# Kernel optimization log

Hardware: AMD Instinct MI355X
Metric: run time of the kernel (lower is better)

Reference implementation:

```python
import jax, jax.numpy as jnp
import numpy as np

EMBED_DIM = 1024
NUM_HEADS = 16
HEAD_DIM = EMBED_DIM // NUM_HEADS
LN_EPS = 1e-5


def setup_inputs() -> dict:
    key = jax.random.key(0)
    ks = jax.random.split(key, 6)
    b, s, d = 2, 2048, EMBED_DIM
    scale = 1.0 / np.sqrt(d)
    x = jax.random.normal(ks[0], (b, s, d), dtype=jnp.float32)
    w_qkv = jax.random.normal(ks[1], (d, 3 * d), dtype=jnp.float32) * scale
    b_qkv = jax.random.normal(ks[2], (3 * d,), dtype=jnp.float32) * 0.02
    w_out = jax.random.normal(ks[3], (d, d), dtype=jnp.float32) * scale
    b_out = jax.random.normal(ks[4], (d,), dtype=jnp.float32) * 0.02
    gamma = jnp.ones((d,), dtype=jnp.float32)
    ln_beta = jnp.zeros((d,), dtype=jnp.float32)
    beta = jax.random.normal(ks[5], (), dtype=jnp.float32) * 0.1
    return {"x": x, "w_qkv": w_qkv, "b_qkv": b_qkv, "w_out": w_out,
            "b_out": b_out, "gamma": gamma, "ln_beta": ln_beta, "beta": beta}


def _layernorm(x, gamma, ln_beta):
    mu = jnp.mean(x, axis=-1, keepdims=True)
    var = jnp.mean(jnp.square(x - mu), axis=-1, keepdims=True)
    return (x - mu) * jax.lax.rsqrt(var + LN_EPS) * gamma + ln_beta


def reference(x, w_qkv, b_qkv, w_out, b_out, gamma, ln_beta, beta):
    b, s, d = x.shape
    h, hd = NUM_HEADS, HEAD_DIM
    residual = x
    xn = _layernorm(x, gamma, ln_beta)
    qkv = xn @ w_qkv + b_qkv                       # [b, s, 3d]
    qkv = qkv.reshape(b, s, 3, h, hd)
    q = jnp.transpose(qkv[:, :, 0], (0, 2, 1, 3))  # [b, h, s, hd]
    k = jnp.transpose(qkv[:, :, 1], (0, 2, 1, 3))
    v = jnp.transpose(qkv[:, :, 2], (0, 2, 1, 3))
    attn = jnp.einsum('bhqd,bhkd->bhqk', q, k) / np.sqrt(hd)
    idx = jnp.arange(s)
    dist = jnp.abs(idx[None, :] - idx[:, None]).astype(attn.dtype)  # [s, s]
    attn = attn + beta * jnp.log1p(dist)[None, None, :, :]
    probs = jax.nn.softmax(attn, axis=-1)
    ctx = jnp.einsum('bhqk,bhkd->bhqd', probs, v)  # [b, h, s, hd]
    ctx = jnp.transpose(ctx, (0, 2, 1, 3)).reshape(b, s, d)
    return residual + ctx @ w_out + b_out
```

## Files before the change

kernel.cpp:

```cpp
#include <hip/hip_runtime.h>

#define SEQ 2048
#define DIM 1024
#define NHEAD 16
#define HDIM 64
#define NTOK 4096
#define N3D 3072

typedef __attribute__((ext_vector_type(8))) short bf16x8;
typedef __attribute__((ext_vector_type(4))) short bf16x4;
typedef __attribute__((ext_vector_type(4))) float floatx4;
typedef __attribute__((ext_vector_type(4))) unsigned short ushortx4;
typedef __attribute__((ext_vector_type(2))) int intx2;

__device__ __forceinline__ unsigned short f2bf(float f) {
    unsigned int u = __builtin_bit_cast(unsigned int, f);
    u += 0x7FFFu + ((u >> 16) & 1u);
    return (unsigned short)(u >> 16);
}

__device__ __forceinline__ unsigned int pack_bf16(float a, float b) {
    return (unsigned int)f2bf(a) | ((unsigned int)f2bf(b) << 16);
}

__device__ __forceinline__ void async_copy16(const void* g, const void* l) {
    __builtin_amdgcn_global_load_lds(
        (const __attribute__((address_space(1))) unsigned int*)(unsigned long long)g,
        (__attribute__((address_space(3))) unsigned int*)(unsigned int)(unsigned long long)l,
        16, 0, 0);
}

#define MFMA_BF16(a, b, c) __builtin_amdgcn_mfma_f32_16x16x32_bf16((a), (b), (c), 0, 0, 0)
#define MFMA16(a, b, c) __builtin_amdgcn_mfma_f32_16x16x16bf16_1k((a), (b), (c), 0, 0, 0)

__global__ __launch_bounds__(256)
void transpose_cvt(const float* __restrict__ src, unsigned short* __restrict__ dst,
                   int rows, int cols) {
    __shared__ float tile[32][33];
    const int c0 = blockIdx.x * 32, r0 = blockIdx.y * 32;
    const int tx = threadIdx.x & 31, ty = threadIdx.x >> 5;
    for (int i = 0; i < 4; ++i) {
        int r = ty + i * 8;
        tile[r][tx] = src[(size_t)(r0 + r) * cols + c0 + tx];
    }
    __syncthreads();
    for (int i = 0; i < 4; ++i) {
        int rr = ty + i * 8;
        dst[(size_t)(c0 + rr) * rows + r0 + tx] = f2bf(tile[tx][rr]);
    }
}

__global__ __launch_bounds__(256)
void ln_kernel(const float* __restrict__ x, const float* __restrict__ gamma,
               const float* __restrict__ lnb, unsigned short* __restrict__ xn) {
    const int row = blockIdx.x;
    const int tid = threadIdx.x;
    const float* xr = x + (size_t)row * DIM;
    float4 v = ((const float4*)xr)[tid];
    float s = v.x + v.y + v.z + v.w;
    float s2 = v.x * v.x + v.y * v.y + v.z * v.z + v.w * v.w;
    for (int off = 1; off < 64; off <<= 1) {
        s += __shfl_xor(s, off, 64);
        s2 += __shfl_xor(s2, off, 64);
    }
    __shared__ float red[8];
    const int wave = tid >> 6, lane = tid & 63;
    if (lane == 0) { red[wave] = s; red[4 + wave] = s2; }
    __syncthreads();
    s = red[0] + red[1] + red[2] + red[3];
    s2 = red[4] + red[5] + red[6] + red[7];
    const float mu = s * (1.0f / DIM);
    const float var = s2 * (1.0f / DIM) - mu * mu;
    const float rstd = rsqrtf(var + 1e-5f);
    float4 g = ((const float4*)gamma)[tid];
    float4 bb = ((const float4*)lnb)[tid];
    unsigned short* o = xn + (size_t)row * DIM + tid * 4;
    o[0] = f2bf((v.x - mu) * rstd * g.x + bb.x);
    o[1] = f2bf((v.y - mu) * rstd * g.y + bb.y);
    o[2] = f2bf((v.z - mu) * rstd * g.z + bb.z);
    o[3] = f2bf((v.w - mu) * rstd * g.w + bb.w);
}

__global__ __launch_bounds__(256)
void qkv_gemm(const unsigned short* __restrict__ A, const unsigned short* __restrict__ Bt,
              const float* __restrict__ bias, unsigned short* __restrict__ qo,
              unsigned short* __restrict__ ko, unsigned short* __restrict__ vTo) {
    __shared__ unsigned short Asm[128 * 32];
    __shared__ unsigned short Bsm[128 * 32];
    const int tid = threadIdx.x;
    const int wave = tid >> 6, lane = tid & 63;
    const int quad = lane >> 4, r16 = lane & 15;
    const int m0 = blockIdx.y * 128, n0 = blockIdx.x * 128;
    const int wm = (wave & 1) * 64, wn = (wave >> 1) * 64;
    floatx4 acc[4][4] = {};
    for (int k0 = 0; k0 < DIM; k0 += 32) {
        __syncthreads();
        for (int p = 0; p < 2; ++p) {
            int s = tid + p * 256;
            int r = s >> 2, c8 = (s & 3) << 3;
            async_copy16(A + (size_t)(m0 + r) * DIM + k0 + c8, Asm + s * 8);
            async_copy16(Bt + (size_t)(n0 + r) * DIM + k0 + c8, Bsm + s * 8);
        }
        __syncthreads();
        bf16x8 af[4], bfr[4];
        for (int i = 0; i < 4; ++i)
            af[i] = *(const bf16x8*)(Asm + (wm + i * 16 + r16) * 32 + quad * 8);
        for (int j = 0; j < 4; ++j)
            bfr[j] = *(const bf16x8*)(Bsm + (wn + j * 16 + r16) * 32 + quad * 8);
        for (int i = 0; i < 4; ++i)
            for (int j = 0; j < 4; ++j)
                acc[i][j] = MFMA_BF16(af[i], bfr[j], acc[i][j]);
    }
    for (int j = 0; j < 4; ++j) {
        int n = n0 + wn + j * 16 + r16;
        float bn = bias[n];
        int part = n >> 10, nn = n & 1023;
        int head = nn >> 6, hdi = nn & 63;
        for (int i = 0; i < 4; ++i) {
            int mbase = m0 + wm + i * 16 + quad * 4;
            int bIdx = mbase >> 11, sIdx = mbase & 2047;
            if (part == 2) {
                ushortx4 pack;
                for (int e = 0; e < 4; ++e) pack[e] = f2bf(acc[i][j][e] + bn);
                *(ushortx4*)(vTo + ((size_t)(bIdx * NHEAD + head) * HDIM + hdi) * SEQ + sIdx) = pack;
            } else {
                unsigned short* dst = (part == 0) ? qo : ko;
                for (int e = 0; e < 4; ++e)
                    dst[((size_t)(bIdx * NHEAD + head) * SEQ + sIdx + e) * HDIM + hdi] =
                        f2bf(acc[i][j][e] + bn);
            }
        }
    }
}

__global__ __launch_bounds__(256)
void attn_kernel(const unsigned short* __restrict__ qg, const unsigned short* __restrict__ kg,
                 const unsigned short* __restrict__ vTg, const float* __restrict__ betap,
                 unsigned short* __restrict__ ctx) {
    __shared__ unsigned short Kd[2][64 * 64];
    __shared__ unsigned short Vd[2][64 * 64];
    __shared__ float2 L2t[SEQ];

    const int tid = threadIdx.x;
    const int wave = tid >> 6, lane = tid & 63;
    const int quad = lane >> 4, r16 = lane & 15;
    const int bh = blockIdx.y, qt = blockIdx.x;
    const int qBase = qt * 128;
    const float betaV = betap[0];
    const float L2E = 1.44269504f;
    const float c1 = 0.125f * L2E;

    for (int t = tid; t < SEQ; t += 256) {
        float fa = betaV * log1pf((float)t) * L2E - 20.0f;
        int t1 = (t + 1 < SEQ) ? t + 1 : SEQ - 1;
        float fb = betaV * log1pf((float)t1) * L2E - 20.0f;
        L2t[t] = make_float2(fa, fb);
    }
    const float* Ff = (const float*)L2t;

    bf16x8 qf[2][2];
    {
        const unsigned short* qp0 =
            qg + ((size_t)bh * SEQ + qBase + wave * 32 + r16) * HDIM;
        qf[0][0] = *(const bf16x8*)(qp0 + quad * 8);
        qf[0][1] = *(const bf16x8*)(qp0 + 32 + quad * 8);
        const unsigned short* qp1 = qp0 + 16 * HDIM;
        qf[1][0] = *(const bf16x8*)(qp1 + quad * 8);
        qf[1][1] = *(const bf16x8*)(qp1 + 32 + quad * 8);
    }

    const int sr = tid >> 3;
    const int scg = (tid & 7) ^ (sr & 7);
    const unsigned short* kbh = kg + (size_t)bh * SEQ * HDIM;
    const unsigned short* vbh = vTg + (size_t)bh * HDIM * SEQ;
    async_copy16(kbh + (size_t)sr * HDIM + scg * 8, &Kd[0][tid * 8]);
    async_copy16(kbh + (size_t)(sr + 32) * HDIM + scg * 8, &Kd[0][2048 + tid * 8]);
    async_copy16(vbh + (size_t)sr * SEQ + scg * 8, &Vd[0][tid * 8]);
    async_copy16(vbh + (size_t)(sr + 32) * SEQ + scg * 8, &Vd[0][2048 + tid * 8]);
    __syncthreads();

    const bf16x4 ones4 = {0x3F80, 0x3F80, 0x3F80, 0x3F80};

    floatx4 o[2][4] = {};
    floatx4 o4[2] = {};
    const int qWB0 = qBase + wave * 32;
    const int qrow0 = qWB0 + r16;

    for (int kt0 = 0; kt0 < SEQ; kt0 += 64) {
        const int buf = (kt0 >> 6) & 1;
        if (kt0 + 64 < SEQ) {
            const unsigned short* kp = kbh + (size_t)(kt0 + 64) * HDIM;
            async_copy16(kp + (size_t)sr * HDIM + scg * 8, &Kd[buf ^ 1][tid * 8]);
            async_copy16(kp + (size_t)(sr + 32) * HDIM + scg * 8, &Kd[buf ^ 1][2048 + tid * 8]);
            async_copy16(vbh + (size_t)sr * SEQ + kt0 + 64 + scg * 8, &Vd[buf ^ 1][tid * 8]);
            async_copy16(vbh + (size_t)(sr + 32) * SEQ + kt0 + 64 + scg * 8,
                         &Vd[buf ^ 1][2048 + tid * 8]);
        }

        floatx4 sc[2][4];
        for (int ct = 0; ct < 4; ++ct) {
            int rK = ct * 16 + r16;
            const unsigned short* kb = &Kd[buf][rK * 64];
            bf16x8 kf0 = *(const bf16x8*)(kb + ((quad ^ (rK & 7)) << 3));
            bf16x8 kf1 = *(const bf16x8*)(kb + (((quad ^ 4) ^ (rK & 7)) << 3));
            for (int qn = 0; qn < 2; ++qn) {
                floatx4 z = {0.f, 0.f, 0.f, 0.f};
                z = MFMA_BF16(kf0, qf[qn][0], z);
                z = MFMA_BF16(kf1, qf[qn][1], z);
                sc[qn][ct] = z;
            }
        }
        bf16x4 pk[2][4];
        for (int qn = 0; qn < 2; ++qn) {
            const int qWB = qWB0 + qn * 16;
            const int qrow = qrow0 + qn * 16;
            for (int ct = 0; ct < 4; ++ct) {
                const int keyTile = kt0 + ct * 16;
                const int key0 = keyTile + quad * 4;
                floatx4 s = sc[qn][ct];
                if (qWB >= keyTile + 16) {
                    int dlo = qrow - key0 - 3;
                    float2 a = L2t[dlo], b = L2t[dlo + 2];
                    s[0] = __builtin_amdgcn_exp2f(s[0] * c1 + b.y);
                    s[1] = __builtin_amdgcn_exp2f(s[1] * c1 + b.x);
                    s[2] = __builtin_amdgcn_exp2f(s[2] * c1 + a.y);
                    s[3] = __builtin_amdgcn_exp2f(s[3] * c1 + a.x);
                } else if (keyTile >= qWB + 16) {
                    int dlo = key0 - qrow;
                    float2 a = L2t[dlo], b = L2t[dlo + 2];
                    s[0] = __builtin_amdgcn_exp2f(s[0] * c1 + a.x);
                    s[1] = __builtin_amdgcn_exp2f(s[1] * c1 + a.y);
                    s[2] = __builtin_amdgcn_exp2f(s[2] * c1 + b.x);
                    s[3] = __builtin_amdgcn_exp2f(s[3] * c1 + b.y);
                } else {
                    for (int i = 0; i < 4; ++i) {
                        int d = key0 + i - qrow;
                        d = d < 0 ? -d : d;
                        s[i] = __builtin_amdgcn_exp2f(s[i] * c1 + Ff[2 * d]);
                    }
                }
                intx2 u = {(int)pack_bf16(s[0], s[1]), (int)pack_bf16(s[2], s[3])};
                pk[qn][ct] = __builtin_bit_cast(bf16x4, u);
            }
        }
        for (int ks = 0; ks < 4; ++ks) {
            o4[0] = MFMA16(ones4, pk[0][ks], o4[0]);
            o4[1] = MFMA16(ones4, pk[1][ks], o4[1]);
            for (int nt = 0; nt < 4; ++nt) {
                int rV = nt * 16 + r16;
                const unsigned short* vb = &Vd[buf][rV * 64];
                bf16x4 vf = *(const bf16x4*)(vb +
                    (((ks * 2 + (quad >> 1)) ^ (rV & 7)) << 3) + ((quad & 1) << 2));
                o[0][nt] = MFMA16(vf, pk[0][ks], o[0][nt]);
                o[1][nt] = MFMA16(vf, pk[1][ks], o[1][nt]);
            }
        }
        __syncthreads();
    }

    const int b_ = bh >> 4, h_ = bh & 15;
    for (int qn = 0; qn < 2; ++qn) {
        float inv = 1.0f / o4[qn][0];
        int q = qBase + wave * 32 + qn * 16 + r16;
        size_t base = ((size_t)(b_ * SEQ + q)) * DIM + h_ * HDIM;
        for (int nt = 0; nt < 4; ++nt) {
            ushortx4 pck;
            for (int i = 0; i < 4; ++i) pck[i] = f2bf(o[qn][nt][i] * inv);
            *(ushortx4*)(ctx + base + nt * 16 + quad * 4) = pck;
        }
    }
}

__global__ __launch_bounds__(256)
void out_gemm(const unsigned short* __restrict__ A, const unsigned short* __restrict__ Bt,
              const float* __restrict__ bias, const float* __restrict__ resid,
              float* __restrict__ out) {
    __shared__ unsigned short Asm[128 * 32];
    __shared__ unsigned short Bsm[64 * 32];
    const int tid = threadIdx.x;
    const int wave = tid >> 6, lane = tid & 63;
    const int quad = lane >> 4, r16 = lane & 15;
    const int m0 = blockIdx.y * 128, n0 = blockIdx.x * 64;
    const int wm = (wave & 1) * 64, wn = (wave >> 1) * 32;
    floatx4 acc[4][2] = {};
    for (int k0 = 0; k0 < DIM; k0 += 32) {
        __syncthreads();
        for (int p = 0; p < 2; ++p) {
            int s = tid + p * 256;
            int r = s >> 2, c8 = (s & 3) << 3;
            async_copy16(A + (size_t)(m0 + r) * DIM + k0 + c8, Asm + s * 8);
        }
        {
            int r = tid >> 2, c8 = (tid & 3) << 3;
            async_copy16(Bt + (size_t)(n0 + r) * DIM + k0 + c8, Bsm + tid * 8);
        }
        __syncthreads();
        bf16x8 af[4], bfr[2];
        for (int i = 0; i < 4; ++i)
            af[i] = *(const bf16x8*)(Asm + (wm + i * 16 + r16) * 32 + quad * 8);
        for (int j = 0; j < 2; ++j)
            bfr[j] = *(const bf16x8*)(Bsm + (wn + j * 16 + r16) * 32 + quad * 8);
        for (int i = 0; i < 4; ++i)
            for (int j = 0; j < 2; ++j)
                acc[i][j] = MFMA_BF16(af[i], bfr[j], acc[i][j]);
    }
    for (int i = 0; i < 4; ++i)
        for (int j = 0; j < 2; ++j)
            for (int e = 0; e < 4; ++e) {
                int m = m0 + wm + i * 16 + quad * 4 + e;
                int n = n0 + wn + j * 16 + r16;
                out[(size_t)m * DIM + n] = acc[i][j][e] + bias[n] + resid[(size_t)m * DIM + n];
            }
}

extern "C" void kernel_launch(void* const* d_in, const int* in_sizes, int n_in,
                              void* d_out, int out_size, void* d_ws, size_t ws_size,
                              hipStream_t stream) {
    const float* x     = (const float*)d_in[0];
    const float* w_qkv = (const float*)d_in[1];
    const float* b_qkv = (const float*)d_in[2];
    const float* w_out = (const float*)d_in[3];
    const float* b_out = (const float*)d_in[4];
    const float* gamma = (const float*)d_in[5];
    const float* ln_b  = (const float*)d_in[6];
    const float* beta  = (const float*)d_in[7];
    float* out = (float*)d_out;

    char* ws = (char*)d_ws;
    const size_t MB = 1u << 20;
    unsigned short* xn    = (unsigned short*)(ws);
    unsigned short* wqkvT = (unsigned short*)(ws + 8 * MB);
    unsigned short* woutT = (unsigned short*)(ws + 14 * MB);
    unsigned short* qb    = (unsigned short*)(ws + 16 * MB);
    unsigned short* kb    = (unsigned short*)(ws + 24 * MB);
    unsigned short* vTb   = (unsigned short*)(ws + 32 * MB);
    unsigned short* ctx   = xn;

    transpose_cvt<<<dim3(96, 32), 256, 0, stream>>>(w_qkv, wqkvT, DIM, N3D);
    transpose_cvt<<<dim3(32, 32), 256, 0, stream>>>(w_out, woutT, DIM, DIM);
    ln_kernel<<<NTOK, 256, 0, stream>>>(x, gamma, ln_b, xn);
    qkv_gemm<<<dim3(24, 32), 256, 0, stream>>>(xn, wqkvT, b_qkv, qb, kb, vTb);
    attn_kernel<<<dim3(SEQ / 128, 32), 256, 0, stream>>>(qb, kb, vTb, beta, ctx);
    out_gemm<<<dim3(16, 32), 256, 0, stream>>>(ctx, woutT, b_out, x, out);
}
```

Measured before the change: 247.5 us.

## Split attention key range across two wave groups and precompute bias table globally

After: 275.8 us. 1.11x slower.

```diff
diff --git a/kernel.cpp b/kernel.cpp
--- a/kernel.cpp
+++ b/kernel.cpp
@@ -32,6 +32,18 @@
 
 #define MFMA_BF16(a, b, c) __builtin_amdgcn_mfma_f32_16x16x32_bf16((a), (b), (c), 0, 0, 0)
 #define MFMA16(a, b, c) __builtin_amdgcn_mfma_f32_16x16x16bf16_1k((a), (b), (c), 0, 0, 0)
+
+__global__ __launch_bounds__(256)
+void bias_init(const float* __restrict__ betap, float2* __restrict__ gt) {
+    const int i = blockIdx.x * 256 + threadIdx.x;
+    if (i >= SEQ) return;
+    const float b = betap[0];
+    const float L2E = 1.44269504f;
+    float fa = b * log1pf((float)i) * L2E - 20.0f;
+    int i1 = (i + 1 < SEQ) ? i + 1 : SEQ - 1;
+    float fb = b * log1pf((float)i1) * L2E - 20.0f;
+    gt[i] = make_float2(fa, fb);
+}
 
 __global__ __launch_bounds__(256)
 void transpose_cvt(const float* __restrict__ src, unsigned short* __restrict__ dst,
@@ -133,35 +145,26 @@
     }
 }
 
-__global__ __launch_bounds__(256)
+__global__ __launch_bounds__(512, 4)
 void attn_kernel(const unsigned short* __restrict__ qg, const unsigned short* __restrict__ kg,
-                 const unsigned short* __restrict__ vTg, const float* __restrict__ betap,
+                 const unsigned short* __restrict__ vTg, const float2* __restrict__ gt,
                  unsigned short* __restrict__ ctx) {
-    __shared__ unsigned short Kd[2][64 * 64];
-    __shared__ unsigned short Vd[2][64 * 64];
-    __shared__ float2 L2t[SEQ];
+    __shared__ unsigned short Kd[2][2][4096];
+    __shared__ unsigned short Vd[2][2][4096];
 
     const int tid = threadIdx.x;
     const int wave = tid >> 6, lane = tid & 63;
     const int quad = lane >> 4, r16 = lane & 15;
+    const int grp = wave >> 2, wq = wave & 3;
     const int bh = blockIdx.y, qt = blockIdx.x;
     const int qBase = qt * 128;
-    const float betaV = betap[0];
-    const float L2E = 1.44269504f;
-    const float c1 = 0.125f * L2E;
-
-    for (int t = tid; t < SEQ; t += 256) {
-        float fa = betaV * log1pf((float)t) * L2E - 20.0f;
-        int t1 = (t + 1 < SEQ) ? t + 1 : SEQ - 1;
-        float fb = betaV * log1pf((float)t1) * L2E - 20.0f;
-        L2t[t] = make_float2(fa, fb);
-    }
-    const float* Ff = (const float*)L2t;
+    const float c1 = 0.125f * 1.44269504f;
+    const float* Ffg = (const float*)gt;
 
     bf16x8 qf[2][2];
     {
         const unsigned short* qp0 =
-            qg + ((size_t)bh * SEQ + qBase + wave * 32 + r16) * HDIM;
+            qg + ((size_t)bh * SEQ + qBase + wq * 32 + r16) * HDIM;
         qf[0][0] = *(const bf16x8*)(qp0 + quad * 8);
         qf[0][1] = *(const bf16x8*)(qp0 + 32 + quad * 8);
         const unsigned short* qp1 = qp0 + 16 * HDIM;
@@ -173,34 +176,35 @@
     const int scg = (tid & 7) ^ (sr & 7);
     const unsigned short* kbh = kg + (size_t)bh * SEQ * HDIM;
     const unsigned short* vbh = vTg + (size_t)bh * HDIM * SEQ;
-    async_copy16(kbh + (size_t)sr * HDIM + scg * 8, &Kd[0][tid * 8]);
-    async_copy16(kbh + (size_t)(sr + 32) * HDIM + scg * 8, &Kd[0][2048 + tid * 8]);
-    async_copy16(vbh + (size_t)sr * SEQ + scg * 8, &Vd[0][tid * 8]);
-    async_copy16(vbh + (size_t)(sr + 32) * SEQ + scg * 8, &Vd[0][2048 + tid * 8]);
+    async_copy16(kbh + (size_t)sr * HDIM + scg * 8, &Kd[0][0][tid * 8]);
+    async_copy16(kbh + (size_t)(1024 + sr) * HDIM + scg * 8, &Kd[1][0][tid * 8]);
+    async_copy16(vbh + (size_t)sr * SEQ + scg * 8, &Vd[0][0][tid * 8]);
+    async_copy16(vbh + (size_t)sr * SEQ + 1024 + scg * 8, &Vd[1][0][tid * 8]);
     __syncthreads();
 
     const bf16x4 ones4 = {0x3F80, 0x3F80, 0x3F80, 0x3F80};
 
     floatx4 o[2][4] = {};
     floatx4 o4[2] = {};
-    const int qWB0 = qBase + wave * 32;
+    const int qWB0 = qBase + wq * 32;
     const int qrow0 = qWB0 + r16;
-
-    for (int kt0 = 0; kt0 < SEQ; kt0 += 64) {
-        const int buf = (kt0 >> 6) & 1;
-        if (kt0 + 64 < SEQ) {
-            const unsigned short* kp = kbh + (size_t)(kt0 + 64) * HDIM;
-            async_copy16(kp + (size_t)sr * HDIM + scg * 8, &Kd[buf ^ 1][tid * 8]);
-            async_copy16(kp + (size_t)(sr + 32) * HDIM + scg * 8, &Kd[buf ^ 1][2048 + tid * 8]);
-            async_copy16(vbh + (size_t)sr * SEQ + kt0 + 64 + scg * 8, &Vd[buf ^ 1][tid * 8]);
-            async_copy16(vbh + (size_t)(sr + 32) * SEQ + kt0 + 64 + scg * 8,
-                         &Vd[buf ^ 1][2048 + tid * 8]);
-        }
+    const int kGrpBase = grp << 10;
+
+    for (int it = 0; it < 16; ++it) {
+        const int buf = it & 1;
+        if (it + 1 < 16) {
+            const int nk = (it + 1) << 6;
+            async_copy16(kbh + (size_t)(nk + sr) * HDIM + scg * 8, &Kd[0][buf ^ 1][tid * 8]);
+            async_copy16(kbh + (size_t)(1024 + nk + sr) * HDIM + scg * 8, &Kd[1][buf ^ 1][tid * 8]);
+            async_copy16(vbh + (size_t)sr * SEQ + nk + scg * 8, &Vd[0][buf ^ 1][tid * 8]);
+            async_copy16(vbh + (size_t)sr * SEQ + 1024 + nk + scg * 8, &Vd[1][buf ^ 1][tid * 8]);
+        }
+        const int kt0 = kGrpBase + (it << 6);
 
         floatx4 sc[2][4];
         for (int ct = 0; ct < 4; ++ct) {
             int rK = ct * 16 + r16;
-            const unsigned short* kb = &Kd[buf][rK * 64];
+            const unsigned short* kb = &Kd[grp][buf][rK * 64];
             bf16x8 kf0 = *(const bf16x8*)(kb + ((quad ^ (rK & 7)) << 3));
             bf16x8 kf1 = *(const bf16x8*)(kb + (((quad ^ 4) ^ (rK & 7)) << 3));
             for (int qn = 0; qn < 2; ++qn) {
@@ -220,14 +224,14 @@
                 floatx4 s = sc[qn][ct];
                 if (qWB >= keyTile + 16) {
                     int dlo = qrow - key0 - 3;
-                    float2 a = L2t[dlo], b = L2t[dlo + 2];
+                    float2 a = gt[dlo], b = gt[dlo + 2];
                     s[0] = __builtin_amdgcn_exp2f(s[0] * c1 + b.y);
                     s[1] = __builtin_amdgcn_exp2f(s[1] * c1 + b.x);
                     s[2] = __builtin_amdgcn_exp2f(s[2] * c1 + a.y);
                     s[3] = __builtin_amdgcn_exp2f(s[3] * c1 + a.x);
                 } else if (keyTile >= qWB + 16) {
                     int dlo = key0 - qrow;
-                    float2 a = L2t[dlo], b = L2t[dlo + 2];
+                    float2 a = gt[dlo], b = gt[dlo + 2];
                     s[0] = __builtin_amdgcn_exp2f(s[0] * c1 + a.x);
                     s[1] = __builtin_amdgcn_exp2f(s[1] * c1 + a.y);
                     s[2] = __builtin_amdgcn_exp2f(s[2] * c1 + b.x);
@@ -236,7 +240,7 @@
                     for (int i = 0; i < 4; ++i) {
                         int d = key0 + i - qrow;
                         d = d < 0 ? -d : d;
-                        s[i] = __builtin_amdgcn_exp2f(s[i] * c1 + Ff[2 * d]);
+                        s[i] = __builtin_amdgcn_exp2f(s[i] * c1 + Ffg[2 * d]);
                     }
                 }
                 intx2 u = {(int)pack_bf16(s[0], s[1]), (int)pack_bf16(s[2], s[3])};
@@ -248,7 +252,7 @@
             o4[1] = MFMA16(ones4, pk[1][ks], o4[1]);
             for (int nt = 0; nt < 4; ++nt) {
                 int rV = nt * 16 + r16;
-                const unsigned short* vb = &Vd[buf][rV * 64];
+                const unsigned short* vb = &Vd[grp][buf][rV * 64];
                 bf16x4 vf = *(const bf16x4*)(vb +
                     (((ks * 2 + (quad >> 1)) ^ (rV & 7)) << 3) + ((quad & 1) << 2));
                 o[0][nt] = MFMA16(vf, pk[0][ks], o[0][nt]);
@@ -258,15 +262,32 @@
         __syncthreads();
     }
 
-    const int b_ = bh >> 4, h_ = bh & 15;
-    for (int qn = 0; qn < 2; ++qn) {
-        float inv = 1.0f / o4[qn][0];
-        int q = qBase + wave * 32 + qn * 16 + r16;
-        size_t base = ((size_t)(b_ * SEQ + q)) * DIM + h_ * HDIM;
-        for (int nt = 0; nt < 4; ++nt) {
-            ushortx4 pck;
-            for (int i = 0; i < 4; ++i) pck[i] = f2bf(o[qn][nt][i] * inv);
-            *(ushortx4*)(ctx + base + nt * 16 + quad * 4) = pck;
+    float* KdF = (float*)Kd;
+    float* VdF = (float*)Vd;
+    if (grp == 1) {
+        const int base = wq * 2048 + lane * 32;
+        for (int qn = 0; qn < 2; ++qn)
+            for (int nt = 0; nt < 4; ++nt)
+                *(floatx4*)(KdF + base + (qn * 4 + nt) * 4) = o[qn][nt];
+        VdF[wq * 128 + lane * 2 + 0] = o4[0][0];
+        VdF[wq * 128 + lane * 2 + 1] = o4[1][0];
+    }
+    __syncthreads();
+    if (grp == 0) {
+        const int base = wq * 2048 + lane * 32;
+        const int b_ = bh >> 4, h_ = bh & 15;
+        for (int qn = 0; qn < 2; ++qn) {
+            float l = o4[qn][0] + VdF[wq * 128 + lane * 2 + qn];
+            float inv = 1.0f / l;
+            int q = qBase + wq * 32 + qn * 16 + r16;
+            size_t obase = ((size_t)(b_ * SEQ + q)) * DIM + h_ * HDIM;
+            for (int nt = 0; nt < 4; ++nt) {
+                floatx4 add = *(const floatx4*)(KdF + base + (qn * 4 + nt) * 4);
+                floatx4 t = o[qn][nt] + add;
+                ushortx4 pck;
+                for (int i = 0; i < 4; ++i) pck[i] = f2bf(t[i] * inv);
+                *(ushortx4*)(ctx + obase + nt * 16 + quad * 4) = pck;
+            }
         }
     }
 }
@@ -334,12 +355,14 @@
     unsigned short* qb    = (unsigned short*)(ws + 16 * MB);
     unsigned short* kb    = (unsigned short*)(ws + 24 * MB);
     unsigned short* vTb   = (unsigned short*)(ws + 32 * MB);
+    float2*         gt    = (float2*)(ws + 40 * MB);
     unsigned short* ctx   = xn;
 
+    bias_init<<<dim3(8), 256, 0, stream>>>(beta, gt);
     transpose_cvt<<<dim3(96, 32), 256, 0, stream>>>(w_qkv, wqkvT, DIM, N3D);
     transpose_cvt<<<dim3(32, 32), 256, 0, stream>>>(w_out, woutT, DIM, DIM);
     ln_kernel<<<NTOK, 256, 0, stream>>>(x, gamma, ln_b, xn);
     qkv_gemm<<<dim3(24, 32), 256, 0, stream>>>(xn, wqkvT, b_qkv, qb, kb, vTb);
-    attn_kernel<<<dim3(SEQ / 128, 32), 256, 0, stream>>>(qb, kb, vTb, beta, ctx);
+    attn_kernel<<<dim3(SEQ / 128, 32), 512, 0, stream>>>(qb, kb, vTb, gt, ctx);
     out_gemm<<<dim3(16, 32), 256, 0, stream>>>(ctx, woutT, b_out, x, out);
 }
```

## Split attention keys in two halves and combine partial outputs

Applied to the files above, without the earlier changes.

After: 237.0 us. 4.3% less time.

```diff
diff --git a/kernel.cpp b/kernel.cpp
--- a/kernel.cpp
+++ b/kernel.cpp
@@ -133,30 +133,26 @@
     }
 }
 
-__global__ __launch_bounds__(256)
+__global__ __launch_bounds__(256, 4)
 void attn_kernel(const unsigned short* __restrict__ qg, const unsigned short* __restrict__ kg,
                  const unsigned short* __restrict__ vTg, const float* __restrict__ betap,
-                 unsigned short* __restrict__ ctx) {
-    __shared__ unsigned short Kd[2][64 * 64];
-    __shared__ unsigned short Vd[2][64 * 64];
-    __shared__ float2 L2t[SEQ];
+                 unsigned short* __restrict__ opart, float* __restrict__ lpart) {
+    __shared__ unsigned short Kd[2][4096];
+    __shared__ unsigned short Vd[2][4096];
+    __shared__ float Ff[SEQ];
 
     const int tid = threadIdx.x;
     const int wave = tid >> 6, lane = tid & 63;
     const int quad = lane >> 4, r16 = lane & 15;
-    const int bh = blockIdx.y, qt = blockIdx.x;
+    const int bh = blockIdx.y, qt = blockIdx.x, ks = blockIdx.z;
     const int qBase = qt * 128;
+    const int kBase = ks << 10;
     const float betaV = betap[0];
     const float L2E = 1.44269504f;
     const float c1 = 0.125f * L2E;
 
-    for (int t = tid; t < SEQ; t += 256) {
-        float fa = betaV * log1pf((float)t) * L2E - 20.0f;
-        int t1 = (t + 1 < SEQ) ? t + 1 : SEQ - 1;
-        float fb = betaV * log1pf((float)t1) * L2E - 20.0f;
-        L2t[t] = make_float2(fa, fb);
-    }
-    const float* Ff = (const float*)L2t;
+    for (int t = tid; t < SEQ; t += 256)
+        Ff[t] = betaV * log1pf((float)t) * L2E - 20.0f;
 
     bf16x8 qf[2][2];
     {
@@ -173,10 +169,10 @@
     const int scg = (tid & 7) ^ (sr & 7);
     const unsigned short* kbh = kg + (size_t)bh * SEQ * HDIM;
     const unsigned short* vbh = vTg + (size_t)bh * HDIM * SEQ;
-    async_copy16(kbh + (size_t)sr * HDIM + scg * 8, &Kd[0][tid * 8]);
-    async_copy16(kbh + (size_t)(sr + 32) * HDIM + scg * 8, &Kd[0][2048 + tid * 8]);
-    async_copy16(vbh + (size_t)sr * SEQ + scg * 8, &Vd[0][tid * 8]);
-    async_copy16(vbh + (size_t)(sr + 32) * SEQ + scg * 8, &Vd[0][2048 + tid * 8]);
+    async_copy16(kbh + (size_t)(kBase + sr) * HDIM + scg * 8, &Kd[0][tid * 8]);
+    async_copy16(kbh + (size_t)(kBase + sr + 32) * HDIM + scg * 8, &Kd[0][2048 + tid * 8]);
+    async_copy16(vbh + (size_t)sr * SEQ + kBase + scg * 8, &Vd[0][tid * 8]);
+    async_copy16(vbh + (size_t)(sr + 32) * SEQ + kBase + scg * 8, &Vd[0][2048 + tid * 8]);
     __syncthreads();
 
     const bf16x4 ones4 = {0x3F80, 0x3F80, 0x3F80, 0x3F80};
@@ -186,15 +182,15 @@
     const int qWB0 = qBase + wave * 32;
     const int qrow0 = qWB0 + r16;
 
-    for (int kt0 = 0; kt0 < SEQ; kt0 += 64) {
-        const int buf = (kt0 >> 6) & 1;
-        if (kt0 + 64 < SEQ) {
-            const unsigned short* kp = kbh + (size_t)(kt0 + 64) * HDIM;
-            async_copy16(kp + (size_t)sr * HDIM + scg * 8, &Kd[buf ^ 1][tid * 8]);
-            async_copy16(kp + (size_t)(sr + 32) * HDIM + scg * 8, &Kd[buf ^ 1][2048 + tid * 8]);
-            async_copy16(vbh + (size_t)sr * SEQ + kt0 + 64 + scg * 8, &Vd[buf ^ 1][tid * 8]);
-            async_copy16(vbh + (size_t)(sr + 32) * SEQ + kt0 + 64 + scg * 8,
-                         &Vd[buf ^ 1][2048 + tid * 8]);
+    for (int it = 0; it < 16; ++it) {
+        const int buf = it & 1;
+        const int kt0 = kBase + (it << 6);
+        if (it + 1 < 16) {
+            const int nk = kt0 + 64;
+            async_copy16(kbh + (size_t)(nk + sr) * HDIM + scg * 8, &Kd[buf ^ 1][tid * 8]);
+            async_copy16(kbh + (size_t)(nk + sr + 32) * HDIM + scg * 8, &Kd[buf ^ 1][2048 + tid * 8]);
+            async_copy16(vbh + (size_t)sr * SEQ + nk + scg * 8, &Vd[buf ^ 1][tid * 8]);
+            async_copy16(vbh + (size_t)(sr + 32) * SEQ + nk + scg * 8, &Vd[buf ^ 1][2048 + tid * 8]);
         }
 
         floatx4 sc[2][4];
@@ -219,56 +215,73 @@
                 const int key0 = keyTile + quad * 4;
                 floatx4 s = sc[qn][ct];
                 if (qWB >= keyTile + 16) {
-                    int dlo = qrow - key0 - 3;
-                    float2 a = L2t[dlo], b = L2t[dlo + 2];
-                    s[0] = __builtin_amdgcn_exp2f(s[0] * c1 + b.y);
-                    s[1] = __builtin_amdgcn_exp2f(s[1] * c1 + b.x);
-                    s[2] = __builtin_amdgcn_exp2f(s[2] * c1 + a.y);
-                    s[3] = __builtin_amdgcn_exp2f(s[3] * c1 + a.x);
+                    const float* lp = &Ff[qrow - key0 - 3];
+                    for (int i = 0; i < 4; ++i)
+                        s[i] = __builtin_amdgcn_exp2f(s[i] * c1 + lp[3 - i]);
                 } else if (keyTile >= qWB + 16) {
-                    int dlo = key0 - qrow;
-                    float2 a = L2t[dlo], b = L2t[dlo + 2];
-                    s[0] = __builtin_amdgcn_exp2f(s[0] * c1 + a.x);
-                    s[1] = __builtin_amdgcn_exp2f(s[1] * c1 + a.y);
-                    s[2] = __builtin_amdgcn_exp2f(s[2] * c1 + b.x);
-                    s[3] = __builtin_amdgcn_exp2f(s[3] * c1 + b.y);
+                    const float* lp = &Ff[key0 - qrow];
+                    for (int i = 0; i < 4; ++i)
+                        s[i] = __builtin_amdgcn_exp2f(s[i] * c1 + lp[i]);
                 } else {
                     for (int i = 0; i < 4; ++i) {
                         int d = key0 + i - qrow;
                         d = d < 0 ? -d : d;
-                        s[i] = __builtin_amdgcn_exp2f(s[i] * c1 + Ff[2 * d]);
+                        s[i] = __builtin_amdgcn_exp2f(s[i] * c1 + Ff[d]);
                     }
                 }
                 intx2 u = {(int)pack_bf16(s[0], s[1]), (int)pack_bf16(s[2], s[3])};
                 pk[qn][ct] = __builtin_bit_cast(bf16x4, u);
             }
         }
-        for (int ks = 0; ks < 4; ++ks) {
-            o4[0] = MFMA16(ones4, pk[0][ks], o4[0]);
-            o4[1] = MFMA16(ones4, pk[1][ks], o4[1]);
+        for (int kss = 0; kss < 4; ++kss) {
+            o4[0] = MFMA16(ones4, pk[0][kss], o4[0]);
+            o4[1] = MFMA16(ones4, pk[1][kss], o4[1]);
             for (int nt = 0; nt < 4; ++nt) {
                 int rV = nt * 16 + r16;
                 const unsigned short* vb = &Vd[buf][rV * 64];
                 bf16x4 vf = *(const bf16x4*)(vb +
-                    (((ks * 2 + (quad >> 1)) ^ (rV & 7)) << 3) + ((quad & 1) << 2));
-                o[0][nt] = MFMA16(vf, pk[0][ks], o[0][nt]);
-                o[1][nt] = MFMA16(vf, pk[1][ks], o[1][nt]);
-            }
-        }
-        __syncthreads();
-    }
-
+                    (((kss * 2 + (quad >> 1)) ^ (rV & 7)) << 3) + ((quad & 1) << 2));
+                o[0][nt] = MFMA16(vf, pk[0][kss], o[0][nt]);
+                o[1][nt] = MFMA16(vf, pk[1][kss], o[1][nt]);
+            }
+        }
+        __syncthreads();
+    }
+
+    unsigned short* op = opart + (size_t)ks * NTOK * DIM;
     const int b_ = bh >> 4, h_ = bh & 15;
     for (int qn = 0; qn < 2; ++qn) {
-        float inv = 1.0f / o4[qn][0];
         int q = qBase + wave * 32 + qn * 16 + r16;
-        size_t base = ((size_t)(b_ * SEQ + q)) * DIM + h_ * HDIM;
+        size_t rowoff = ((size_t)(b_ * SEQ + q)) * DIM + h_ * HDIM;
         for (int nt = 0; nt < 4; ++nt) {
             ushortx4 pck;
-            for (int i = 0; i < 4; ++i) pck[i] = f2bf(o[qn][nt][i] * inv);
-            *(ushortx4*)(ctx + base + nt * 16 + quad * 4) = pck;
-        }
-    }
+            for (int i = 0; i < 4; ++i) pck[i] = f2bf(o[qn][nt][i]);
+            *(ushortx4*)(op + rowoff + nt * 16 + quad * 4) = pck;
+        }
+        if (quad == 0)
+            lpart[(size_t)ks * NHEAD * 2 * SEQ + (size_t)bh * SEQ + q] = o4[qn][0];
+    }
+}
+
+__global__ __launch_bounds__(256)
+void attn_combine(const unsigned short* __restrict__ oA, unsigned short* __restrict__ oB,
+                  const float* __restrict__ lA, const float* __restrict__ lB) {
+    const int row = blockIdx.x;
+    const int col = threadIdx.x * 4;
+    const int b_ = row >> 11, q = row & 2047;
+    const int head = col >> 6;
+    const int li = (b_ * NHEAD + head) * SEQ + q;
+    const float inv = 1.0f / (lA[li] + lB[li]);
+    const size_t off = (size_t)row * DIM + col;
+    ushortx4 a = *(const ushortx4*)(oA + off);
+    ushortx4 b = *(const ushortx4*)(oB + off);
+    ushortx4 r;
+    for (int i = 0; i < 4; ++i) {
+        float fa = __builtin_bit_cast(float, (unsigned int)(unsigned short)a[i] << 16);
+        float fb = __builtin_bit_cast(float, (unsigned int)(unsigned short)b[i] << 16);
+        r[i] = f2bf((fa + fb) * inv);
+    }
+    *(ushortx4*)(oB + off) = r;
 }
 
 __global__ __launch_bounds__(256)
@@ -329,17 +342,20 @@
     char* ws = (char*)d_ws;
     const size_t MB = 1u << 20;
     unsigned short* xn    = (unsigned short*)(ws);
-    unsigned short* wqkvT = (unsigned short*)(ws + 8 * MB);
-    unsigned short* woutT = (unsigned short*)(ws + 14 * MB);
-    unsigned short* qb    = (unsigned short*)(ws + 16 * MB);
-    unsigned short* kb    = (unsigned short*)(ws + 24 * MB);
-    unsigned short* vTb   = (unsigned short*)(ws + 32 * MB);
-    unsigned short* ctx   = xn;
+    unsigned short* oA    = (unsigned short*)(ws);
+    unsigned short* oB    = (unsigned short*)(ws + 8 * MB);
+    unsigned short* wqkvT = (unsigned short*)(ws + 16 * MB);
+    float*          lprt  = (float*)(ws + 16 * MB);
+    unsigned short* woutT = (unsigned short*)(ws + 22 * MB);
+    unsigned short* qb    = (unsigned short*)(ws + 24 * MB);
+    unsigned short* kb    = (unsigned short*)(ws + 32 * MB);
+    unsigned short* vTb   = (unsigned short*)(ws + 40 * MB);
 
     transpose_cvt<<<dim3(96, 32), 256, 0, stream>>>(w_qkv, wqkvT, DIM, N3D);
     transpose_cvt<<<dim3(32, 32), 256, 0, stream>>>(w_out, woutT, DIM, DIM);
     ln_kernel<<<NTOK, 256, 0, stream>>>(x, gamma, ln_b, xn);
     qkv_gemm<<<dim3(24, 32), 256, 0, stream>>>(xn, wqkvT, b_qkv, qb, kb, vTb);
-    attn_kernel<<<dim3(SEQ / 128, 32), 256, 0, stream>>>(qb, kb, vTb, beta, ctx);
-    out_gemm<<<dim3(16, 32), 256, 0, stream>>>(ctx, woutT, b_out, x, out);
-}
+    attn_kernel<<<dim3(SEQ / 128, 32, 2), 256, 0, stream>>>(qb, kb, vTb, beta, oA, lprt);
+    attn_combine<<<NTOK, 256, 0, stream>>>(oA, oB, lprt, lprt + 32 * SEQ);
+    out_gemm<<<dim3(16, 32), 256, 0, stream>>>(oB, woutT, b_out, x, out);
+}
```
